# Optimization experiments

Hardware: AMD Instinct MI355X
Metric: run time of the kernel (lower is better)

The kernel has to match this reference:

```python
import jax, jax.numpy as jnp
import numpy as np

EMBED_DIM = 1024
NUM_HEADS = 16
HEAD_DIM = EMBED_DIM // NUM_HEADS


def setup_inputs() -> dict:
    key = jax.random.key(0)
    ks = jax.random.split(key, 9)
    B, S, D = 2, 2048, EMBED_DIM
    scale = 1.0 / np.sqrt(D)
    x = jax.random.normal(ks[0], (B, S, D), dtype=jnp.float32)
    mask = jnp.ones((B, S), dtype=jnp.int32)
    # nn.Linear weights: [out_features, in_features]
    Wq = jax.random.normal(ks[1], (D, D), dtype=jnp.float32) * scale
    bq = jnp.zeros((D,), dtype=jnp.float32)
    Wk = jax.random.normal(ks[2], (D, D), dtype=jnp.float32) * scale
    bk = jnp.zeros((D,), dtype=jnp.float32)
    Wv = jax.random.normal(ks[3], (D, D), dtype=jnp.float32) * scale
    bv = jnp.zeros((D,), dtype=jnp.float32)
    Wo = jax.random.normal(ks[4], (D, D), dtype=jnp.float32) * scale
    bo = jnp.zeros((D,), dtype=jnp.float32)
    return {"x": x, "mask": mask, "Wq": Wq, "bq": bq, "Wk": Wk, "bk": bk,
            "Wv": Wv, "bv": bv, "Wo": Wo, "bo": bo}


def reference(x, mask, Wq, bq, Wk, bk, Wv, bv, Wo, bo):
    B, S, D = x.shape
    H, Hd = NUM_HEADS, HEAD_DIM
    q = (x @ Wq.T + bq).reshape(B, S, H, Hd).transpose(0, 2, 1, 3)  # [B,H,S,Hd]
    k = (x @ Wk.T + bk).reshape(B, S, H, Hd).transpose(0, 2, 1, 3)
    v = (x @ Wv.T + bv).reshape(B, S, H, Hd).transpose(0, 2, 1, 3)
    scores = jnp.einsum('bhqd,bhkd->bhqk', q, k) / jnp.sqrt(jnp.float32(Hd))
    m = mask[:, None, None, :]  # [B,1,1,S]
    scores = jnp.where(m == 0, jnp.float32(-1e9), scores)
    attn = jax.nn.softmax(scores, axis=-1)  # dropout p=0 / eval -> identity
    out = jnp.einsum('bhqk,bhkd->bhqd', attn, v)
    out = out.transpose(0, 2, 1, 3).reshape(B, S, D)
    return out @ Wo.T + bo
```

## Files before the change

kernel.cpp:

```cpp
#include <hip/hip_runtime.h>


typedef unsigned short u16;
typedef unsigned int   u32;
typedef __bf16 bf16;
typedef bf16 bf16x8 __attribute__((ext_vector_type(8)));
typedef float f32x4  __attribute__((ext_vector_type(4)));
typedef float f32x16 __attribute__((ext_vector_type(16)));
typedef u16  u16x8  __attribute__((ext_vector_type(8)));
typedef u16  u16x4  __attribute__((ext_vector_type(4)));
typedef u32  u32x4  __attribute__((ext_vector_type(4)));

#define DEV __device__ __forceinline__

#if __has_builtin(__builtin_amdgcn_exp2f)
#define EXP2(x) __builtin_amdgcn_exp2f(x)
#else
#define EXP2(x) exp2f(x)
#endif

DEV void gld_lds16(const void* g, void* l) {
  __builtin_amdgcn_global_load_lds(
      (__attribute__((address_space(1))) void*)(const_cast<void*>(g)),
      (__attribute__((address_space(3))) void*)(l), 16, 0, 0);
}

DEV u16 f2bf(float f) {
  u32 u = __builtin_bit_cast(u32, f);
  u32 lsb = (u >> 16) & 1u;
  u += 0x7fffu + lsb;
  return (u16)(u >> 16);
}

DEV float bf2f(u16 u) {
  u32 v = ((u32)u) << 16;
  return __builtin_bit_cast(float, v);
}

DEV u32 pbf2(float lo, float hi) {
  u32 d;
  asm("v_cvt_pk_bf16_f32 %0, %1, %2" : "=v"(d) : "v"(lo), "v"(hi));
  return d;
}

DEV void pl32swap(u32& a, u32& b) {
  asm("v_permlane32_swap_b32 %0, %1" : "+v"(a), "+v"(b));
}

struct CastArgs {
  const float* src[5];
  u16* dst[5];
  int n4[5];
};

__global__ __launch_bounds__(256) void cast_f32_bf16_kernel(CastArgs a) {
  const int y = blockIdx.y;
  const float4* s = (const float4*)a.src[y];
  u16x4* d = (u16x4*)a.dst[y];
  const int n4 = a.n4[y];
  const int stride = gridDim.x * blockDim.x;
  for (int i = blockIdx.x * blockDim.x + threadIdx.x; i < n4; i += stride) {
    float4 f = s[i];
    u16x4 o;
    o[0] = f2bf(f.x); o[1] = f2bf(f.y); o[2] = f2bf(f.z); o[3] = f2bf(f.w);
    d[i] = o;
  }
}

template<bool OUTF32>
__global__ __launch_bounds__(256, 3) void gemm_nt_kernel(
    const u16* __restrict__ A,
    const u16* __restrict__ B0, const u16* __restrict__ B1, const u16* __restrict__ B2,
    const float* __restrict__ bias0, const float* __restrict__ bias1, const float* __restrict__ bias2,
    void* __restrict__ C0, void* __restrict__ C1, void* __restrict__ C2,
    int M, int N, int K, float alpha0, float alpha1, float alpha2)
{
  __shared__ __attribute__((aligned(16))) u16 As[2][4096];
  __shared__ __attribute__((aligned(16))) u16 Bs[2][4096];

  const int z = blockIdx.z;
  const u16* Bmat   = (z == 0) ? B0 : (z == 1) ? B1 : B2;
  const float* bias = (z == 0) ? bias0 : (z == 1) ? bias1 : bias2;
  void* Cout        = (z == 0) ? C0 : (z == 1) ? C1 : C2;
  const float alpha = (z == 0) ? alpha0 : (z == 1) ? alpha1 : alpha2;

  const int tid  = threadIdx.x;
  const int lane = tid & 63;
  const int w    = tid >> 6;
  const int wr   = w >> 1, wc = w & 1;
  const int l15  = lane & 15, l4 = lane >> 4;
  const int m0   = blockIdx.y * 128;
  const int n0   = blockIdx.x * 128;

  const int u0 = tid;
  const int u1 = tid + 256;
  const int r0 = u0 >> 2, c0s = (u0 & 3) ^ (r0 & 3);
  const int r1 = u1 >> 2, c1s = (u1 & 3) ^ (r1 & 3);
  const size_t K2 = (size_t)K * 2;
  const char* pa0 = (const char*)A + (size_t)(m0 + r0) * K2 + c0s * 16;
  const char* pa1 = (const char*)A + (size_t)(m0 + r1) * K2 + c1s * 16;
  const char* pb0 = (const char*)Bmat + (size_t)(n0 + r0) * K2 + c0s * 16;
  const char* pb1 = (const char*)Bmat + (size_t)(n0 + r1) * K2 + c1s * 16;

  f32x4 acc[4][4] = {};

  const int aoff0 = (wr * 64 + l15) * 64 + ((l4 ^ (l15 & 3)) * 16);
  const int boff0 = (wc * 64 + l15) * 64 + ((l4 ^ (l15 & 3)) * 16);

  gld_lds16(pa0, (char*)As[0] + u0 * 16);
  gld_lds16(pa1, (char*)As[0] + u1 * 16);
  gld_lds16(pb0, (char*)Bs[0] + u0 * 16);
  gld_lds16(pb1, (char*)Bs[0] + u1 * 16);
  __syncthreads();

  int buf = 0;
  for (int k0 = 0; k0 < K; k0 += 32) {
    if (k0 + 32 < K) {
      const size_t ko = (size_t)(k0 + 32) * 2;
      gld_lds16(pa0 + ko, (char*)As[buf ^ 1] + u0 * 16);
      gld_lds16(pa1 + ko, (char*)As[buf ^ 1] + u1 * 16);
      gld_lds16(pb0 + ko, (char*)Bs[buf ^ 1] + u0 * 16);
      gld_lds16(pb1 + ko, (char*)Bs[buf ^ 1] + u1 * 16);
    }
    bf16x8 af[4], bfr[4];
#pragma unroll
    for (int mt = 0; mt < 4; ++mt)
      af[mt] = *(const bf16x8*)((const char*)As[buf] + aoff0 + mt * 16 * 64);
#pragma unroll
    for (int nt = 0; nt < 4; ++nt)
      bfr[nt] = *(const bf16x8*)((const char*)Bs[buf] + boff0 + nt * 16 * 64);
#pragma unroll
    for (int mt = 0; mt < 4; ++mt)
#pragma unroll
      for (int nt = 0; nt < 4; ++nt)
        acc[mt][nt] = __builtin_amdgcn_mfma_f32_16x16x32_bf16(af[mt], bfr[nt], acc[mt][nt], 0, 0, 0);
    __syncthreads();
    buf ^= 1;
  }

  if (!OUTF32 && z == 2) {
#pragma unroll
    for (int nt = 0; nt < 4; ++nt) {
      const int col = n0 + wc * 64 + nt * 16 + l15;
      const float bv = bias[col];
#pragma unroll
      for (int mt = 0; mt < 4; ++mt) {
        const int row0 = m0 + wr * 64 + mt * 16 + l4 * 4;
        const int b = row0 >> 11, s0 = row0 & 2047;
        u16x4 o;
#pragma unroll
        for (int r = 0; r < 4; ++r) o[r] = f2bf(acc[mt][nt][r] + bv);
        *(u16x4*)((u16*)Cout + (size_t)b * 2097152 + (size_t)col * 2048 + s0) = o;
      }
    }
  } else {
#pragma unroll
    for (int nt = 0; nt < 4; ++nt) {
      const int col = n0 + wc * 64 + nt * 16 + l15;
      const float bv = bias[col];
#pragma unroll
      for (int mt = 0; mt < 4; ++mt) {
        const int row = m0 + wr * 64 + mt * 16 + l4 * 4;
#pragma unroll
        for (int r = 0; r < 4; ++r) {
          float v = (acc[mt][nt][r] + bv) * alpha;
          if (OUTF32) ((float*)Cout)[(size_t)(row + r) * N + col] = v;
          else        ((u16*)Cout)[(size_t)(row + r) * N + col] = f2bf(v);
        }
      }
    }
  }
}

template<int SPLIT>
__global__ __launch_bounds__(256, 4) void attn_fwd_kernel(
    const u16* __restrict__ Qg, const u16* __restrict__ Kg, const u16* __restrict__ Vtg,
    const int* __restrict__ maskg, u16* __restrict__ Og,
    u16* __restrict__ Opart, float* __restrict__ Lpart)
{
  __shared__ __attribute__((aligned(16))) u16 lds[17408];
  __shared__ u32 tzb[4];

  const int tid  = threadIdx.x;
  const int lane = tid & 63;
  const int w    = tid >> 6;
  const int l31  = lane & 31, half = lane >> 5;
  const int qt   = blockIdx.x;
  const int bh   = blockIdx.y;
  const int zh   = (SPLIT == 2) ? blockIdx.z : 0;
  const int b    = bh >> 4, h = bh & 15;
  const int qbase = qt * 128 + w * 32;
  const int NT   = 32 / SPLIT;
  const int kt0  = zh * NT;

  {
    const int4* mp = (const int4*)(maskg + b * 2048 + tid * 8);
    const int4 a = mp[0], c = mp[1];
    const bool az = (a.x == 0) | (a.y == 0) | (a.z == 0) | (a.w == 0) |
                    (c.x == 0) | (c.y == 0) | (c.z == 0) | (c.w == 0);
    const unsigned long long bal = __ballot(az);
    if (lane == 0) {
      u32 bits = 0;
#pragma unroll
      for (int t = 0; t < 8; ++t)
        if ((bal >> (8 * t)) & 0xFFull) bits |= (1u << t);
      tzb[w] = bits;
    }
  }

  const int u0 = tid, u1 = tid + 256;
  const int r0 = u0 >> 3, c0 = (u0 & 7) ^ (r0 & 7);
  const int r1 = u1 >> 3, c1 = (u1 & 7) ^ (r1 & 7);
  const char* kp0 = (const char*)Kg + ((size_t)(b * 2048 + kt0 * 64 + r0) * 1024 + h * 64 + c0 * 8) * 2;
  const char* kp1 = (const char*)Kg + ((size_t)(b * 2048 + kt0 * 64 + r1) * 1024 + h * 64 + c1 * 8) * 2;
  const char* vp0 = (const char*)Vtg + ((size_t)b * 2097152 + (size_t)h * 131072 + (size_t)r0 * 2048 + (kt0 * 64 + c0 * 8)) * 2;
  const char* vp1 = (const char*)Vtg + ((size_t)b * 2097152 + (size_t)h * 131072 + (size_t)r1 * 2048 + (kt0 * 64 + c1 * 8)) * 2;

  bf16x8 qf[4];
  {
    const char* qrow = (const char*)Qg + ((size_t)(b * 2048 + qbase + l31) * 1024 + h * 64) * 2;
#pragma unroll
    for (int c = 0; c < 4; ++c)
      qf[c] = *(const bf16x8*)(qrow + c * 32 + half * 16);
  }

  bf16x8 ones;
#pragma unroll
  for (int i = 0; i < 8; ++i) ones[i] = (bf16)1.0f;

  const int* mrow_ptr = maskg + b * 2048;

  gld_lds16(kp0, (char*)lds + u0 * 16);
  gld_lds16(kp1, (char*)lds + u1 * 16);
  gld_lds16(vp0, (char*)(lds + 8192) + u0 * 16);
  gld_lds16(vp1, (char*)(lds + 8192) + u1 * 16);
  __syncthreads();

  const u32 tilezero = tzb[0] | (tzb[1] << 8) | (tzb[2] << 16) | (tzb[3] << 24);

  f32x16 oT[2] = {};
  f32x16 lacc = {};

  int buf = 0;
  for (int i = 0; i < NT; ++i) {
    const int kt = kt0 + i;
    if (i < NT - 1) {
      const size_t ko = (size_t)(i + 1) * 131072;
      const size_t vo = (size_t)(i + 1) * 128;
      gld_lds16(kp0 + ko, (char*)(lds + (buf ^ 1) * 4096) + u0 * 16);
      gld_lds16(kp1 + ko, (char*)(lds + (buf ^ 1) * 4096) + u1 * 16);
      gld_lds16(vp0 + vo, (char*)(lds + 8192 + (buf ^ 1) * 4096) + u0 * 16);
      gld_lds16(vp1 + vo, (char*)(lds + 8192 + (buf ^ 1) * 4096) + u1 * 16);
    }

    const char* ktile = (const char*)(lds + buf * 4096);
    const char* vtile = (const char*)(lds + 8192 + buf * 4096);

#pragma unroll
    for (int sub = 0; sub < 2; ++sub) {
      f32x16 st = {};
      const int krow = sub * 32 + l31;
      const char* kbase = ktile + krow * 128;
#pragma unroll
      for (int c = 0; c < 4; ++c) {
        bf16x8 kf = *(const bf16x8*)(kbase + (((c * 2 + half) ^ (krow & 7)) * 16));
        st = __builtin_amdgcn_mfma_f32_32x32x16_bf16(kf, qf[c], st, 0, 0, 0);
      }

      if (tilezero & (1u << kt)) {
        const int kvb = kt * 64 + sub * 32 + half * 4;
#pragma unroll
        for (int r = 0; r < 16; ++r)
          if (mrow_ptr[kvb + (r & 3) + 8 * (r >> 2)] == 0) st[r] = -1e9f;
      }

#pragma unroll
      for (int r = 0; r < 16; ++r)
        st[r] = EXP2(st[r] - 8.0f);

      u32 a0 = pbf2(st[0], st[1]),   b0 = pbf2(st[4], st[5]);
      u32 a1 = pbf2(st[2], st[3]),   b1 = pbf2(st[6], st[7]);
      u32 a2 = pbf2(st[8], st[9]),   b2 = pbf2(st[12], st[13]);
      u32 a3 = pbf2(st[10], st[11]), b3 = pbf2(st[14], st[15]);
      pl32swap(a0, b0); pl32swap(a1, b1); pl32swap(a2, b2); pl32swap(a3, b3);
      u32x4 wlo = {a0, a1, b0, b1}, whi = {a2, a3, b2, b3};
      bf16x8 Blo = __builtin_bit_cast(bf16x8, wlo);
      bf16x8 Bhi = __builtin_bit_cast(bf16x8, whi);

      lacc = __builtin_amdgcn_mfma_f32_32x32x16_bf16(ones, Blo, lacc, 0, 0, 0);
      lacc = __builtin_amdgcn_mfma_f32_32x32x16_bf16(ones, Bhi, lacc, 0, 0, 0);

#pragma unroll
      for (int hdt = 0; hdt < 2; ++hdt) {
        const int vrow = hdt * 32 + l31;
        const char* vbase = vtile + vrow * 128;
        bf16x8 vlo = *(const bf16x8*)(vbase + (((sub * 4 + half) ^ (vrow & 7)) * 16));
        bf16x8 vhi = *(const bf16x8*)(vbase + (((sub * 4 + 2 + half) ^ (vrow & 7)) * 16));
        oT[hdt] = __builtin_amdgcn_mfma_f32_32x32x16_bf16(vlo, Blo, oT[hdt], 0, 0, 0);
        oT[hdt] = __builtin_amdgcn_mfma_f32_32x32x16_bf16(vhi, Bhi, oT[hdt], 0, 0, 0);
      }
    }

    __syncthreads();
    buf ^= 1;
  }

  const float ltot = lacc[0];

  if constexpr (SPLIT == 1) {
    const float inv = 1.0f / ltot;
    u16* sc = lds + w * 2304;
#pragma unroll
    for (int hdt = 0; hdt < 2; ++hdt)
#pragma unroll
      for (int run = 0; run < 4; ++run) {
        u16x4 o4;
#pragma unroll
        for (int i = 0; i < 4; ++i) o4[i] = f2bf(oT[hdt][run * 4 + i] * inv);
        const int hd0 = hdt * 32 + run * 8 + half * 4;
        *(u16x4*)(sc + l31 * 72 + hd0) = o4;
      }
    __syncthreads();
#pragma unroll
    for (int rep = 0; rep < 4; ++rep) {
      const int q = rep * 8 + (lane >> 3);
      u16x8 v = *(const u16x8*)(sc + q * 72 + (lane & 7) * 8);
      const size_t tok = (size_t)(b * 2048 + qbase + q);
      *(u16x8*)(Og + tok * 1024 + h * 64 + (lane & 7) * 8) = v;
    }
  } else {
    if (lane < 32)
      Lpart[(size_t)zh * 65536 + (size_t)(b * 2048 + qbase + l31) * 16 + h] = ltot;
    float* scf = (float*)lds + w * 2112;
#pragma unroll
    for (int hdt = 0; hdt < 2; ++hdt)
#pragma unroll
      for (int r = 0; r < 16; ++r) {
        const int hd = hdt * 32 + (r & 3) + 8 * (r >> 2) + 4 * half;
        scf[hd * 33 + l31] = oT[hdt][r];
      }
    __syncthreads();
#pragma unroll
    for (int rep = 0; rep < 8; ++rep) {
      const int qloc = rep * 4 + (lane >> 4);
      const int hd0 = (lane & 15) * 4;
      u16x4 o;
#pragma unroll
      for (int j = 0; j < 4; ++j) o[j] = f2bf(scf[(hd0 + j) * 33 + qloc]);
      const size_t tok = (size_t)(b * 2048 + qbase + qloc);
      *(u16x4*)(Opart + (size_t)zh * 4194304 + tok * 1024 + h * 64 + hd0) = o;
    }
  }
}

__global__ __launch_bounds__(256) void attn_combine_kernel(
    const u16* __restrict__ Opart, const float* __restrict__ Lpart,
    u16* __restrict__ Ob)
{
  const int idx = blockIdx.x * 256 + threadIdx.x;
  const int tok = idx >> 8;
  const int c4  = (idx & 255) * 4;
  const int h   = c4 >> 6;
  u16x4 a = *(const u16x4*)(Opart + (size_t)tok * 1024 + c4);
  u16x4 b = *(const u16x4*)(Opart + 4194304 + (size_t)tok * 1024 + c4);
  const float l = Lpart[tok * 16 + h] + Lpart[65536 + tok * 16 + h];
  const float inv = 1.0f / l;
  u16x4 o;
#pragma unroll
  for (int j = 0; j < 4; ++j) o[j] = f2bf((bf2f(a[j]) + bf2f(b[j])) * inv);
  *(u16x4*)(Ob + (size_t)tok * 1024 + c4) = o;
}

extern "C" void kernel_launch(void* const* d_in, const int* in_sizes, int n_in,
                              void* d_out, int out_size, void* d_ws, size_t ws_size,
                              hipStream_t stream) {
  const float* x  = (const float*)d_in[0];
  const int* mask = (const int*)d_in[1];
  const float* Wq = (const float*)d_in[2];
  const float* bq = (const float*)d_in[3];
  const float* Wk = (const float*)d_in[4];
  const float* bk = (const float*)d_in[5];
  const float* Wv = (const float*)d_in[6];
  const float* bv = (const float*)d_in[7];
  const float* Wo = (const float*)d_in[8];
  const float* bo = (const float*)d_in[9];
  float* out = (float*)d_out;

  const int Mtok = 2 * 2048;
  const int D = 1024;

  const size_t base_need = (size_t)Mtok * D * 2 * 5 + (size_t)D * D * 2 * 4;
  const size_t split_extra = (size_t)2 * Mtok * D * 2 + (size_t)2 * Mtok * 16 * 4;
  if (ws_size < base_need) return;
  const bool do_split = ws_size >= base_need + split_extra;

  char* p = (char*)d_ws;
  u16* xb  = (u16*)p; p += (size_t)Mtok * D * 2;
  u16* wqb = (u16*)p; p += (size_t)D * D * 2;
  u16* wkb = (u16*)p; p += (size_t)D * D * 2;
  u16* wvb = (u16*)p; p += (size_t)D * D * 2;
  u16* wob = (u16*)p; p += (size_t)D * D * 2;
  u16* Qb  = (u16*)p; p += (size_t)Mtok * D * 2;
  u16* Kb  = (u16*)p; p += (size_t)Mtok * D * 2;
  u16* Vtb = (u16*)p; p += (size_t)Mtok * D * 2;
  u16* Ob  = (u16*)p; p += (size_t)Mtok * D * 2;
  u16* Opart = (u16*)p; p += (size_t)2 * Mtok * D * 2;
  float* Lpart = (float*)p; p += (size_t)2 * Mtok * 16 * 4;

  CastArgs ca;
  ca.src[0] = x;  ca.dst[0] = xb;  ca.n4[0] = Mtok * D / 4;
  ca.src[1] = Wq; ca.dst[1] = wqb; ca.n4[1] = D * D / 4;
  ca.src[2] = Wk; ca.dst[2] = wkb; ca.n4[2] = D * D / 4;
  ca.src[3] = Wv; ca.dst[3] = wvb; ca.n4[3] = D * D / 4;
  ca.src[4] = Wo; ca.dst[4] = wob; ca.n4[4] = D * D / 4;
  cast_f32_bf16_kernel<<<dim3(256, 5), 256, 0, stream>>>(ca);

  const float qalpha = 0.125f * 1.44269504088896340736f;
  gemm_nt_kernel<false><<<dim3(D / 128, Mtok / 128, 3), 256, 0, stream>>>(
      xb, wqb, wkb, wvb, bq, bk, bv, Qb, Kb, Vtb, Mtok, D, D, qalpha, 1.0f, 1.0f);

  if (do_split) {
    attn_fwd_kernel<2><<<dim3(2048 / 128, 32, 2), 256, 0, stream>>>(
        Qb, Kb, Vtb, mask, Ob, Opart, Lpart);
    attn_combine_kernel<<<Mtok * D / 4 / 256, 256, 0, stream>>>(Opart, Lpart, Ob);
  } else {
    attn_fwd_kernel<1><<<dim3(2048 / 128, 32, 1), 256, 0, stream>>>(
        Qb, Kb, Vtb, mask, Ob, Opart, Lpart);
  }

  gemm_nt_kernel<true><<<dim3(D / 128, Mtok / 128, 1), 256, 0, stream>>>(
      Ob, wob, wob, wob, bo, bo, bo, out, out, out, Mtok, D, D, 1.0f, 1.0f, 1.0f);
}
```

Baseline: 125.1 us.

## Triple-buffer K/V tiles in attention with prefetch distance two

Replaces the double-buffered K/V LDS pipeline with a three-stage ring buffer that prefetches two tiles ahead. It uses explicit vmcnt waits and a single barrier per iteration in place of the trailing __syncthreads. The aim is to hide more global-load latency behind the MFMA work. In exchange LDS grows from about 34KB to 48KB and the launch-bounds occupancy hint drops from 4 to 3 blocks per CU, which may reduce latency hiding across blocks.

Measured after the change: 129.4 us. +3.5%, slower.

```diff
diff --git a/kernel.cpp b/kernel.cpp
--- a/kernel.cpp
+++ b/kernel.cpp
@@ -173,12 +173,12 @@
 }
 
 template<int SPLIT>
-__global__ __launch_bounds__(256, 4) void attn_fwd_kernel(
+__global__ __launch_bounds__(256, 3) void attn_fwd_kernel(
     const u16* __restrict__ Qg, const u16* __restrict__ Kg, const u16* __restrict__ Vtg,
     const int* __restrict__ maskg, u16* __restrict__ Og,
     u16* __restrict__ Opart, float* __restrict__ Lpart)
 {
-  __shared__ __attribute__((aligned(16))) u16 lds[17408];
+  __shared__ __attribute__((aligned(16))) u16 lds[24576];
   __shared__ u32 tzb[4];
 
   const int tid  = threadIdx.x;
@@ -232,8 +232,14 @@
 
   gld_lds16(kp0, (char*)lds + u0 * 16);
   gld_lds16(kp1, (char*)lds + u1 * 16);
-  gld_lds16(vp0, (char*)(lds + 8192) + u0 * 16);
-  gld_lds16(vp1, (char*)(lds + 8192) + u1 * 16);
+  gld_lds16(vp0, (char*)lds + 24576 + u0 * 16);
+  gld_lds16(vp1, (char*)lds + 24576 + u1 * 16);
+  if (NT > 1) {
+    gld_lds16(kp0 + 131072, (char*)lds + 8192 + u0 * 16);
+    gld_lds16(kp1 + 131072, (char*)lds + 8192 + u1 * 16);
+    gld_lds16(vp0 + 128, (char*)lds + 24576 + 8192 + u0 * 16);
+    gld_lds16(vp1 + 128, (char*)lds + 24576 + 8192 + u1 * 16);
+  }
   __syncthreads();
 
   const u32 tilezero = tzb[0] | (tzb[1] << 8) | (tzb[2] << 16) | (tzb[3] << 24);
@@ -241,20 +247,30 @@
   f32x16 oT[2] = {};
   f32x16 lacc = {};
 
-  int buf = 0;
+  int cur = 0;
   for (int i = 0; i < NT; ++i) {
     const int kt = kt0 + i;
-    if (i < NT - 1) {
-      const size_t ko = (size_t)(i + 1) * 131072;
-      const size_t vo = (size_t)(i + 1) * 128;
-      gld_lds16(kp0 + ko, (char*)(lds + (buf ^ 1) * 4096) + u0 * 16);
-      gld_lds16(kp1 + ko, (char*)(lds + (buf ^ 1) * 4096) + u1 * 16);
-      gld_lds16(vp0 + vo, (char*)(lds + 8192 + (buf ^ 1) * 4096) + u0 * 16);
-      gld_lds16(vp1 + vo, (char*)(lds + 8192 + (buf ^ 1) * 4096) + u1 * 16);
-    }
-
-    const char* ktile = (const char*)(lds + buf * 4096);
-    const char* vtile = (const char*)(lds + 8192 + buf * 4096);
+
+    if (i + 1 < NT) {
+      asm volatile("s_waitcnt vmcnt(4)" ::: "memory");
+    } else {
+      asm volatile("s_waitcnt vmcnt(0)" ::: "memory");
+    }
+    __builtin_amdgcn_s_barrier();
+    __builtin_amdgcn_sched_barrier(0);
+
+    if (i + 2 < NT) {
+      const int nb = (cur >= 1) ? cur - 1 : 2;
+      const size_t ko = (size_t)(i + 2) * 131072;
+      const size_t vo = (size_t)(i + 2) * 128;
+      gld_lds16(kp0 + ko, (char*)lds + nb * 8192 + u0 * 16);
+      gld_lds16(kp1 + ko, (char*)lds + nb * 8192 + u1 * 16);
+      gld_lds16(vp0 + vo, (char*)lds + 24576 + nb * 8192 + u0 * 16);
+      gld_lds16(vp1 + vo, (char*)lds + 24576 + nb * 8192 + u1 * 16);
+    }
+
+    const char* ktile = (const char*)lds + cur * 8192;
+    const char* vtile = (const char*)lds + 24576 + cur * 8192;
 
 #pragma unroll
     for (int sub = 0; sub < 2; ++sub) {
@@ -301,9 +317,10 @@
       }
     }
 
-    __syncthreads();
-    buf ^= 1;
-  }
+    cur = (cur == 2) ? 0 : cur + 1;
+  }
+
+  __syncthreads();
 
   const float ltot = lacc[0];
 
```
